# Kernel tuning notes

Measured on AMD Instinct MI355X. Metric: run time of the kernel, lower is better.

## Reference

```python
import jax, jax.numpy as jnp
import numpy as np

EMBED_DIM = 128
NUM_HEADS = 4
HEAD_DIM = EMBED_DIM // NUM_HEADS
B, S = 2, 1024


def setup_inputs() -> dict:
    key = jax.random.key(0)
    ks = jax.random.split(key, 9)
    sc = 1.0 / np.sqrt(EMBED_DIM)
    x = jax.random.normal(ks[0], (B, S, EMBED_DIM), dtype=jnp.float32)
    # torch nn.Linear weights: (out_features, in_features)
    Wq = jax.random.uniform(ks[1], (EMBED_DIM, EMBED_DIM), jnp.float32, -sc, sc)
    bq = jax.random.uniform(ks[2], (EMBED_DIM,), jnp.float32, -sc, sc)
    Wk = jax.random.uniform(ks[3], (EMBED_DIM, EMBED_DIM), jnp.float32, -sc, sc)
    bk = jax.random.uniform(ks[4], (EMBED_DIM,), jnp.float32, -sc, sc)
    Wv = jax.random.uniform(ks[5], (EMBED_DIM, EMBED_DIM), jnp.float32, -sc, sc)
    bv = jax.random.uniform(ks[6], (EMBED_DIM,), jnp.float32, -sc, sc)
    Wo = jax.random.uniform(ks[7], (EMBED_DIM, EMBED_DIM), jnp.float32, -sc, sc)
    bo = jax.random.uniform(ks[8], (EMBED_DIM,), jnp.float32, -sc, sc)
    return {"x": x, "Wq": Wq, "bq": bq, "Wk": Wk, "bk": bk,
            "Wv": Wv, "bv": bv, "Wo": Wo, "bo": bo}


def _heads(y):
    # (B,S,E) -> (B,H,S,D)
    return y.reshape(B, S, NUM_HEADS, HEAD_DIM).transpose(0, 2, 1, 3)


def reference(x, Wq, bq, Wk, bk, Wv, bv, Wo, bo):
    q = _heads(x @ Wq.T + bq)  # (B,H,S,D)
    k = _heads(x @ Wk.T + bk)
    v = _heads(x @ Wv.T + bv)
    # ultrametric (Chebyshev / max-abs) distance: (B,H,S,S)
    dist = jnp.max(jnp.abs(q[:, :, :, None, :] - k[:, :, None, :, :]), axis=-1)
    attn = jax.nn.softmax(-dist, axis=-1)
    attended = jnp.einsum('bhst,bhtd->bhsd', attn, v)
    attended = attended.transpose(0, 2, 1, 3).reshape(B, S, EMBED_DIM)
    return attended @ Wo.T + bo
```

## Files before the change

### kernel.cpp

```cpp
#include <hip/hip_runtime.h>
#include <hip/hip_bf16.h>

#define B_ 2
#define S_ 1024
#define E_ 128
#define H_ 4
#define D_ 32
#define BHSD (B_ * H_ * S_ * D_)
#define LOG2E 1.44269504088896f

__global__ __launch_bounds__(128) void qkv_kernel(
    const float* __restrict__ x,
    const float* __restrict__ Wq, const float* __restrict__ bq,
    const float* __restrict__ Wk, const float* __restrict__ bk,
    const float* __restrict__ Wv, const float* __restrict__ bv,
    float* __restrict__ ws) {
  const int mat = blockIdx.y;
  const float* W    = (mat == 0) ? Wq : (mat == 1) ? Wk : Wv;
  const float* bias = (mat == 0) ? bq : (mat == 1) ? bk : bv;
  const float scale = (mat == 2) ? 1.0f : LOG2E;
  float* outbase = ws + (size_t)mat * BHSD;

  const int row0 = blockIdx.x * 8;
  const int t = threadIdx.x;

  __shared__ __align__(16) float xs[8 * E_];
  const float4* xg = (const float4*)(x + (size_t)row0 * E_);
  float4* xs4 = (float4*)xs;
  #pragma unroll
  for (int i = 0; i < 2; ++i) xs4[t + i * 128] = xg[t + i * 128];
  __syncthreads();

  const int col = t;
  const float4* W4 = (const float4*)(W + (size_t)col * E_);

  float acc[8];
  #pragma unroll
  for (int r = 0; r < 8; ++r) acc[r] = 0.f;

  #pragma unroll 4
  for (int c4 = 0; c4 < E_ / 4; ++c4) {
    float4 w = W4[c4];
    #pragma unroll
    for (int r = 0; r < 8; ++r) {
      float4 xv = xs4[r * (E_ / 4) + c4];
      acc[r] += xv.x * w.x + xv.y * w.y + xv.z * w.z + xv.w * w.w;
    }
  }

  const float bcol = bias[col];
  const int h = col >> 5, d = col & 31;
  #pragma unroll
  for (int r = 0; r < 8; ++r) {
    int row = row0 + r;
    int b = row >> 10, s = row & 1023;
    outbase[(((size_t)(b * H_ + h)) * S_ + s) * D_ + d] = (acc[r] + bcol) * scale;
  }
}

#define QSTRIDE 36
#define PSTRIDE 68

__global__ __launch_bounds__(256) void attn_kernel(
    const float* __restrict__ qg, const float* __restrict__ kg_,
    const float* __restrict__ vg,
    float* __restrict__ part_o, float* __restrict__ part_l) {
  __shared__ __align__(16) float Qs[64 * QSTRIDE];
  __shared__ __align__(16) float Ks[64 * QSTRIDE];
  __shared__ __align__(16) float Vs[64 * QSTRIDE];
  __shared__ __align__(16) float Ps[64 * PSTRIDE];

  const int bx = blockIdx.x;
  const int kc  = bx & 3;
  const int rtl = (bx >> 2) & 15;
  const int head = bx >> 6;
  const int t = threadIdx.x;
  const int w = t >> 6;
  const int lane = t & 63;
  const int rg = lane >> 3;
  const int kg = lane & 7;

  const float* qbase = qg  + (size_t)head * S_ * D_ + (size_t)rtl * 64 * D_;
  const float* kbase = kg_ + (size_t)head * S_ * D_ + (size_t)kc * 256 * D_;
  const float* vbase = vg  + (size_t)head * S_ * D_ + (size_t)kc * 256 * D_;

  {
    const float4* src = (const float4*)qbase;
    #pragma unroll
    for (int i = 0; i < 2; ++i) {
      int f = t + i * 256;
      int r = f >> 3, c4 = f & 7;
      *(float4*)(Qs + r * QSTRIDE + c4 * 4) = src[f];
    }
  }

  float O[8][4];
  #pragma unroll
  for (int i = 0; i < 8; ++i)
    #pragma unroll
    for (int c = 0; c < 4; ++c) O[i][c] = 0.f;
  float lrow[8];
  #pragma unroll
  for (int i = 0; i < 8; ++i) lrow[i] = 0.f;

  for (int it = 0; it < 4; ++it) {
    {
      const float4* ksrc = (const float4*)(kbase + (size_t)it * 64 * D_);
      const float4* vsrc = (const float4*)(vbase + (size_t)it * 64 * D_);
      #pragma unroll
      for (int i = 0; i < 2; ++i) {
        int f = t + i * 256;
        int r = f >> 3, c4 = f & 7;
        *(float4*)(Ks + r * QSTRIDE + c4 * 4) = ksrc[f];
        *(float4*)(Vs + r * QSTRIDE + c4 * 4) = vsrc[f];
      }
    }
    __syncthreads();

    float dist[8][2];
    #pragma unroll
    for (int i = 0; i < 8; ++i) { dist[i][0] = 0.f; dist[i][1] = 0.f; }

    #pragma unroll 2
    for (int c = 0; c < 8; ++c) {
      float4 qv[8];
      #pragma unroll
      for (int i = 0; i < 8; ++i)
        qv[i] = *(const float4*)(Qs + (rg + 8 * i) * QSTRIDE + c * 4);
      float4 kv[2];
      #pragma unroll
      for (int j = 0; j < 2; ++j)
        kv[j] = *(const float4*)(Ks + (w * 16 + kg + 8 * j) * QSTRIDE + c * 4);
      #pragma unroll
      for (int i = 0; i < 8; ++i) {
        #pragma unroll
        for (int j = 0; j < 2; ++j) {
          float m0 = fmaxf(fabsf(qv[i].x - kv[j].x), fabsf(qv[i].y - kv[j].y));
          float m1 = fmaxf(fabsf(qv[i].z - kv[j].z), fabsf(qv[i].w - kv[j].w));
          dist[i][j] = fmaxf(dist[i][j], fmaxf(m0, m1));
        }
      }
    }

    float pp[8][2];
    #pragma unroll
    for (int i = 0; i < 8; ++i) {
      #pragma unroll
      for (int j = 0; j < 2; ++j) {
        float p = exp2f(-dist[i][j]);
        pp[i][j] = p;
        lrow[i] += p;
      }
    }
    #pragma unroll
    for (int j = 0; j < 2; ++j) {
      float* dst = Ps + (w * 16 + kg + 8 * j) * PSTRIDE + rg * 8;
      *(float4*)(dst + 0) = make_float4(pp[0][j], pp[1][j], pp[2][j], pp[3][j]);
      *(float4*)(dst + 4) = make_float4(pp[4][j], pp[5][j], pp[6][j], pp[7][j]);
    }
    __syncthreads();

    const int tk0 = w * 16;
    #pragma unroll 4
    for (int u = 0; u < 16; ++u) {
      const int tk = tk0 + u;
      float4 pa = *(const float4*)(Ps + tk * PSTRIDE + rg * 8);
      float4 pb = *(const float4*)(Ps + tk * PSTRIDE + rg * 8 + 4);
      float4 vv = *(const float4*)(Vs + tk * QSTRIDE + kg * 4);
      O[0][0] = fmaf(pa.x, vv.x, O[0][0]); O[0][1] = fmaf(pa.x, vv.y, O[0][1]);
      O[0][2] = fmaf(pa.x, vv.z, O[0][2]); O[0][3] = fmaf(pa.x, vv.w, O[0][3]);
      O[1][0] = fmaf(pa.y, vv.x, O[1][0]); O[1][1] = fmaf(pa.y, vv.y, O[1][1]);
      O[1][2] = fmaf(pa.y, vv.z, O[1][2]); O[1][3] = fmaf(pa.y, vv.w, O[1][3]);
      O[2][0] = fmaf(pa.z, vv.x, O[2][0]); O[2][1] = fmaf(pa.z, vv.y, O[2][1]);
      O[2][2] = fmaf(pa.z, vv.z, O[2][2]); O[2][3] = fmaf(pa.z, vv.w, O[2][3]);
      O[3][0] = fmaf(pa.w, vv.x, O[3][0]); O[3][1] = fmaf(pa.w, vv.y, O[3][1]);
      O[3][2] = fmaf(pa.w, vv.z, O[3][2]); O[3][3] = fmaf(pa.w, vv.w, O[3][3]);
      O[4][0] = fmaf(pb.x, vv.x, O[4][0]); O[4][1] = fmaf(pb.x, vv.y, O[4][1]);
      O[4][2] = fmaf(pb.x, vv.z, O[4][2]); O[4][3] = fmaf(pb.x, vv.w, O[4][3]);
      O[5][0] = fmaf(pb.y, vv.x, O[5][0]); O[5][1] = fmaf(pb.y, vv.y, O[5][1]);
      O[5][2] = fmaf(pb.y, vv.z, O[5][2]); O[5][3] = fmaf(pb.y, vv.w, O[5][3]);
      O[6][0] = fmaf(pb.z, vv.x, O[6][0]); O[6][1] = fmaf(pb.z, vv.y, O[6][1]);
      O[6][2] = fmaf(pb.z, vv.z, O[6][2]); O[6][3] = fmaf(pb.z, vv.w, O[6][3]);
      O[7][0] = fmaf(pb.w, vv.x, O[7][0]); O[7][1] = fmaf(pb.w, vv.y, O[7][1]);
      O[7][2] = fmaf(pb.w, vv.z, O[7][2]); O[7][3] = fmaf(pb.w, vv.w, O[7][3]);
    }
    __syncthreads();
  }

  #pragma unroll
  for (int i = 0; i < 8; ++i) {
    lrow[i] += __shfl_xor(lrow[i], 1);
    lrow[i] += __shfl_xor(lrow[i], 2);
    lrow[i] += __shfl_xor(lrow[i], 4);
  }

  float* slbuf = Ps + 64 * 64;
  if (kg == 0) {
    #pragma unroll
    for (int i = 0; i < 8; ++i) slbuf[w * 64 + (rg + 8 * i)] = lrow[i];
  }
  if (w == 1) {
    #pragma unroll
    for (int i = 0; i < 8; ++i)
      *(float4*)(Ks + (rg + 8 * i) * QSTRIDE + kg * 4) =
          make_float4(O[i][0], O[i][1], O[i][2], O[i][3]);
  } else if (w == 2) {
    #pragma unroll
    for (int i = 0; i < 8; ++i)
      *(float4*)(Vs + (rg + 8 * i) * QSTRIDE + kg * 4) =
          make_float4(O[i][0], O[i][1], O[i][2], O[i][3]);
  } else if (w == 3) {
    #pragma unroll
    for (int i = 0; i < 8; ++i)
      *(float4*)(Qs + (rg + 8 * i) * QSTRIDE + kg * 4) =
          make_float4(O[i][0], O[i][1], O[i][2], O[i][3]);
  }
  __syncthreads();

  if (w == 0) {
    const size_t base = ((size_t)(head * 16 + rtl) * 4 + kc) * 64;
    #pragma unroll
    for (int i = 0; i < 8; ++i) {
      const int ar = rg + 8 * i;
      float4 a = *(const float4*)(Ks + ar * QSTRIDE + kg * 4);
      float4 b = *(const float4*)(Vs + ar * QSTRIDE + kg * 4);
      float4 c = *(const float4*)(Qs + ar * QSTRIDE + kg * 4);
      float4 r;
      r.x = O[i][0] + a.x + b.x + c.x;
      r.y = O[i][1] + a.y + b.y + c.y;
      r.z = O[i][2] + a.z + b.z + c.z;
      r.w = O[i][3] + a.w + b.w + c.w;
      *(float4*)(part_o + (base + ar) * 32 + kg * 4) = r;
    }
    if (kg == 0) {
      #pragma unroll
      for (int i = 0; i < 8; ++i) {
        const int ar = rg + 8 * i;
        part_l[base + ar] = slbuf[0 * 64 + ar] + slbuf[1 * 64 + ar] +
                            slbuf[2 * 64 + ar] + slbuf[3 * 64 + ar];
      }
    }
  }
}

__global__ __launch_bounds__(128) void out_kernel(
    const float* __restrict__ part_o, const float* __restrict__ part_l,
    const float* __restrict__ Wo, const float* __restrict__ bo,
    float* __restrict__ out) {
  const int row0 = blockIdx.x * 8;
  const int t = threadIdx.x;

  __shared__ __align__(16) float xs[8 * E_];

  const int e = t;
  const int h = e >> 5, d = e & 31;
  #pragma unroll
  for (int i = 0; i < 8; ++i) {
    const int r = row0 + i;
    const int b = r >> 10, s = r & 1023;
    const int rt = (b * H_ + h) * 16 + (s >> 6);
    const int lrow = s & 63;
    float acc = 0.f, lsum = 0.f;
    #pragma unroll
    for (int kc = 0; kc < 4; ++kc) {
      const size_t base = (size_t)(rt * 4 + kc) * 64 + lrow;
      acc  += part_o[base * 32 + d];
      lsum += part_l[base];
    }
    xs[i * E_ + e] = acc / lsum;
  }
  __syncthreads();

  const int col = t;
  const float4* W4 = (const float4*)(Wo + (size_t)col * E_);
  const float4* xs4 = (const float4*)xs;

  float acc[8];
  #pragma unroll
  for (int r = 0; r < 8; ++r) acc[r] = 0.f;

  #pragma unroll 4
  for (int c4 = 0; c4 < E_ / 4; ++c4) {
    float4 w = W4[c4];
    #pragma unroll
    for (int r = 0; r < 8; ++r) {
      float4 xv = xs4[r * (E_ / 4) + c4];
      acc[r] += xv.x * w.x + xv.y * w.y + xv.z * w.z + xv.w * w.w;
    }
  }

  const float bcol = bo[col];
  #pragma unroll
  for (int r = 0; r < 8; ++r)
    out[(size_t)(row0 + r) * E_ + col] = acc[r] + bcol;
}

extern "C" void kernel_launch(void* const* d_in, const int* in_sizes, int n_in,
                              void* d_out, int out_size, void* d_ws, size_t ws_size,
                              hipStream_t stream) {
  const float* x  = (const float*)d_in[0];
  const float* Wq = (const float*)d_in[1];
  const float* bq = (const float*)d_in[2];
  const float* Wk = (const float*)d_in[3];
  const float* bk = (const float*)d_in[4];
  const float* Wv = (const float*)d_in[5];
  const float* bv = (const float*)d_in[6];
  const float* Wo = (const float*)d_in[7];
  const float* bo = (const float*)d_in[8];
  float* ws  = (float*)d_ws;
  float* out = (float*)d_out;

  float* qd = ws;
  float* kd = ws + (size_t)BHSD;
  float* vd = ws + 2 * (size_t)BHSD;
  float* part_o = ws + 3 * (size_t)BHSD;
  float* part_l = part_o + (size_t)128 * 4 * 64 * 32;

  qkv_kernel<<<dim3((B_ * S_) / 8, 3), 128, 0, stream>>>(x, Wq, bq, Wk, bk, Wv, bv, ws);
  attn_kernel<<<dim3(512), 256, 0, stream>>>(qd, kd, vd, part_o, part_l);
  out_kernel<<<dim3((B_ * S_) / 8), 128, 0, stream>>>(part_o, part_l, Wo, bo, out);
}
```

Baseline: 50.67 us.

## Split attention keys into eight chunks and read V directly from global

Doubles the key-dimension split of the attention kernel, so each block covers 128 keys and the grid grows from 512 to 1024 blocks. V is read from global memory (L1/L2) inside the PV loop instead of being staged in LDS, which removes the Vs buffer. The barrier between writing P and the PV product is dropped, which is safe because each wavefront only reads the P rows it wrote itself. This aims to raise occupancy and parallelism, at the cost of twice as many partial outputs written and then reduced in the output kernel, and uncached-LDS V loads on the critical path.

```diff
diff --git a/kernel.cpp b/kernel.cpp
--- a/kernel.cpp
+++ b/kernel.cpp
@@ -67,13 +67,13 @@
     float* __restrict__ part_o, float* __restrict__ part_l) {
   __shared__ __align__(16) float Qs[64 * QSTRIDE];
   __shared__ __align__(16) float Ks[64 * QSTRIDE];
-  __shared__ __align__(16) float Vs[64 * QSTRIDE];
   __shared__ __align__(16) float Ps[64 * PSTRIDE];
+  __shared__ __align__(16) float sm_l[4 * 64];
 
   const int bx = blockIdx.x;
-  const int kc  = bx & 3;
-  const int rtl = (bx >> 2) & 15;
-  const int head = bx >> 6;
+  const int kc   = bx & 7;
+  const int rtl  = (bx >> 3) & 15;
+  const int head = bx >> 7;
   const int t = threadIdx.x;
   const int w = t >> 6;
   const int lane = t & 63;
@@ -81,16 +81,18 @@
   const int kg = lane & 7;
 
   const float* qbase = qg  + (size_t)head * S_ * D_ + (size_t)rtl * 64 * D_;
-  const float* kbase = kg_ + (size_t)head * S_ * D_ + (size_t)kc * 256 * D_;
-  const float* vbase = vg  + (size_t)head * S_ * D_ + (size_t)kc * 256 * D_;
+  const float* kbase = kg_ + (size_t)head * S_ * D_ + (size_t)kc * 128 * D_;
+  const float* vbase = vg  + (size_t)head * S_ * D_ + (size_t)kc * 128 * D_;
 
   {
-    const float4* src = (const float4*)qbase;
+    const float4* qsrc = (const float4*)qbase;
+    const float4* ksrc = (const float4*)kbase;
     #pragma unroll
     for (int i = 0; i < 2; ++i) {
       int f = t + i * 256;
       int r = f >> 3, c4 = f & 7;
-      *(float4*)(Qs + r * QSTRIDE + c4 * 4) = src[f];
+      *(float4*)(Qs + r * QSTRIDE + c4 * 4) = qsrc[f];
+      *(float4*)(Ks + r * QSTRIDE + c4 * 4) = ksrc[f];
     }
   }
 
@@ -103,20 +105,10 @@
   #pragma unroll
   for (int i = 0; i < 8; ++i) lrow[i] = 0.f;
 
-  for (int it = 0; it < 4; ++it) {
-    {
-      const float4* ksrc = (const float4*)(kbase + (size_t)it * 64 * D_);
-      const float4* vsrc = (const float4*)(vbase + (size_t)it * 64 * D_);
-      #pragma unroll
-      for (int i = 0; i < 2; ++i) {
-        int f = t + i * 256;
-        int r = f >> 3, c4 = f & 7;
-        *(float4*)(Ks + r * QSTRIDE + c4 * 4) = ksrc[f];
-        *(float4*)(Vs + r * QSTRIDE + c4 * 4) = vsrc[f];
-      }
-    }
-    __syncthreads();
-
+  __syncthreads();
+
+  #pragma unroll
+  for (int it = 0; it < 2; ++it) {
     float dist[8][2];
     #pragma unroll
     for (int i = 0; i < 8; ++i) { dist[i][0] = 0.f; dist[i][1] = 0.f; }
@@ -158,15 +150,15 @@
       *(float4*)(dst + 0) = make_float4(pp[0][j], pp[1][j], pp[2][j], pp[3][j]);
       *(float4*)(dst + 4) = make_float4(pp[4][j], pp[5][j], pp[6][j], pp[7][j]);
     }
-    __syncthreads();
-
+
+    const float* vG = vbase + (size_t)(it * 64) * D_ + kg * 4;
     const int tk0 = w * 16;
     #pragma unroll 4
     for (int u = 0; u < 16; ++u) {
       const int tk = tk0 + u;
       float4 pa = *(const float4*)(Ps + tk * PSTRIDE + rg * 8);
       float4 pb = *(const float4*)(Ps + tk * PSTRIDE + rg * 8 + 4);
-      float4 vv = *(const float4*)(Vs + tk * QSTRIDE + kg * 4);
+      float4 vv = *(const float4*)(vG + (size_t)tk * D_);
       O[0][0] = fmaf(pa.x, vv.x, O[0][0]); O[0][1] = fmaf(pa.x, vv.y, O[0][1]);
       O[0][2] = fmaf(pa.x, vv.z, O[0][2]); O[0][3] = fmaf(pa.x, vv.w, O[0][3]);
       O[1][0] = fmaf(pa.y, vv.x, O[1][0]); O[1][1] = fmaf(pa.y, vv.y, O[1][1]);
@@ -184,7 +176,18 @@
       O[7][0] = fmaf(pb.w, vv.x, O[7][0]); O[7][1] = fmaf(pb.w, vv.y, O[7][1]);
       O[7][2] = fmaf(pb.w, vv.z, O[7][2]); O[7][3] = fmaf(pb.w, vv.w, O[7][3]);
     }
+
     __syncthreads();
+    if (it == 0) {
+      const float4* ksrc = (const float4*)(kbase + 64 * D_);
+      #pragma unroll
+      for (int i = 0; i < 2; ++i) {
+        int f = t + i * 256;
+        int r = f >> 3, c4 = f & 7;
+        *(float4*)(Ks + r * QSTRIDE + c4 * 4) = ksrc[f];
+      }
+      __syncthreads();
+    }
   }
 
   #pragma unroll
@@ -194,10 +197,9 @@
     lrow[i] += __shfl_xor(lrow[i], 4);
   }
 
-  float* slbuf = Ps + 64 * 64;
   if (kg == 0) {
     #pragma unroll
-    for (int i = 0; i < 8; ++i) slbuf[w * 64 + (rg + 8 * i)] = lrow[i];
+    for (int i = 0; i < 8; ++i) sm_l[w * 64 + (rg + 8 * i)] = lrow[i];
   }
   if (w == 1) {
     #pragma unroll
@@ -207,24 +209,24 @@
   } else if (w == 2) {
     #pragma unroll
     for (int i = 0; i < 8; ++i)
-      *(float4*)(Vs + (rg + 8 * i) * QSTRIDE + kg * 4) =
+      *(float4*)(Qs + (rg + 8 * i) * QSTRIDE + kg * 4) =
           make_float4(O[i][0], O[i][1], O[i][2], O[i][3]);
   } else if (w == 3) {
     #pragma unroll
     for (int i = 0; i < 8; ++i)
-      *(float4*)(Qs + (rg + 8 * i) * QSTRIDE + kg * 4) =
+      *(float4*)(Ps + (rg + 8 * i) * PSTRIDE + kg * 4) =
           make_float4(O[i][0], O[i][1], O[i][2], O[i][3]);
   }
   __syncthreads();
 
   if (w == 0) {
-    const size_t base = ((size_t)(head * 16 + rtl) * 4 + kc) * 64;
+    const size_t base = ((size_t)((head * 16 + rtl) * 8 + kc)) * 64;
     #pragma unroll
     for (int i = 0; i < 8; ++i) {
       const int ar = rg + 8 * i;
       float4 a = *(const float4*)(Ks + ar * QSTRIDE + kg * 4);
-      float4 b = *(const float4*)(Vs + ar * QSTRIDE + kg * 4);
-      float4 c = *(const float4*)(Qs + ar * QSTRIDE + kg * 4);
+      float4 b = *(const float4*)(Qs + ar * QSTRIDE + kg * 4);
+      float4 c = *(const float4*)(Ps + ar * PSTRIDE + kg * 4);
       float4 r;
       r.x = O[i][0] + a.x + b.x + c.x;
       r.y = O[i][1] + a.y + b.y + c.y;
@@ -236,8 +238,8 @@
       #pragma unroll
       for (int i = 0; i < 8; ++i) {
         const int ar = rg + 8 * i;
-        part_l[base + ar] = slbuf[0 * 64 + ar] + slbuf[1 * 64 + ar] +
-                            slbuf[2 * 64 + ar] + slbuf[3 * 64 + ar];
+        part_l[base + ar] = sm_l[0 * 64 + ar] + sm_l[1 * 64 + ar] +
+                            sm_l[2 * 64 + ar] + sm_l[3 * 64 + ar];
       }
     }
   }
@@ -262,8 +264,8 @@
     const int lrow = s & 63;
     float acc = 0.f, lsum = 0.f;
     #pragma unroll
-    for (int kc = 0; kc < 4; ++kc) {
-      const size_t base = (size_t)(rt * 4 + kc) * 64 + lrow;
+    for (int kc = 0; kc < 8; ++kc) {
+      const size_t base = ((size_t)(rt * 8 + kc)) * 64 + lrow;
       acc  += part_o[base * 32 + d];
       lsum += part_l[base];
     }
@@ -314,9 +316,9 @@
   float* kd = ws + (size_t)BHSD;
   float* vd = ws + 2 * (size_t)BHSD;
   float* part_o = ws + 3 * (size_t)BHSD;
-  float* part_l = part_o + (size_t)128 * 4 * 64 * 32;
+  float* part_l = part_o + (size_t)128 * 8 * 64 * 32;
 
   qkv_kernel<<<dim3((B_ * S_) / 8, 3), 128, 0, stream>>>(x, Wq, bq, Wk, bk, Wv, bv, ws);
-  attn_kernel<<<dim3(512), 256, 0, stream>>>(qd, kd, vd, part_o, part_l);
+  attn_kernel<<<dim3(1024), 256, 0, stream>>>(qd, kd, vd, part_o, part_l);
   out_kernel<<<dim3((B_ * S_) / 8), 128, 0, stream>>>(part_o, part_l, Wo, bo, out);
 }
```

Result: slower. 52.27 us (+3.2%).
